# Performance work log

Hardware: AMD Instinct MI355X
Metric: run time of the kernel (lower is better)

## Reference

```python
import jax, jax.numpy as jnp
import numpy as np

BATCH, C, BOX = 8, 1, 160
N, L = 20, 20


def setup_inputs() -> dict:
    key = jax.random.key(0)
    k1, k2, k3 = jax.random.split(key, 3)
    x = jax.random.normal(k1, (BATCH, C, BOX, BOX), dtype=jnp.float32)
    basis = jax.random.normal(k2, (N, L, 2, BOX, BOX), dtype=jnp.float32)
    angles = jax.random.uniform(k3, (BATCH,), dtype=jnp.float32) * (2.0 * np.pi)
    return {"x": x, "basis": basis, "angles": angles}


def reference(x, basis, angles):
    # euclid2basis: linear basis projection (GEMM in disguise)
    # coeffs: [b, c, N, L, 2]
    coeffs = jnp.einsum('bcij,nlrij->bcnlr', x, basis)

    # rotate: complex rotation of angular modes, angle scaled by harmonic index l
    l_mult = jnp.arange(L, dtype=x.dtype)                  # [L]
    ang = angles[:, None, None, None] * l_mult             # [b, 1, 1, L]
    ca, sa = jnp.cos(ang), jnp.sin(ang)
    a = coeffs[..., 0] * ca + coeffs[..., 1] * sa
    b = coeffs[..., 1] * ca - coeffs[..., 0] * sa
    rot = jnp.stack([a, b], axis=-1)                       # [b, c, N, L, 2]

    # basis2euclid: reconstruction (transpose GEMM)
    out = jnp.einsum('bcnlr,nlrij->bcij', rot, basis)      # [b, c, H, W]
    return out
```

## Files before the change

### kernel.cpp

```cpp
#include <hip/hip_runtime.h>
#include <math.h>

#define BATCH   8
#define LDIM    20
#define PIX     25600
#define PIX4    6400
#define NLPAIRS 400
#define NLR     800

#define KSPLIT  20
#define SLICE   (PIX4 / KSPLIT)
#define WITER   (SLICE / 64)
#define BROWS   8

#define RPIX    64
#define RKS     8
#define RKLEN   (NLR / RKS)

__global__ __launch_bounds__(256) void proj_kernel(
    const float* __restrict__ x,
    const float* __restrict__ basis,
    float* __restrict__ part)
{
    const int tid   = threadIdx.x;
    const int lane  = tid & 63;
    const int wv    = tid >> 6;
    const int r0    = blockIdx.x * BROWS + wv * 2;
    const int kbase = blockIdx.y * SLICE;

    const float4* __restrict__ b0 = (const float4*)(basis + (size_t)r0 * PIX);
    const float4* __restrict__ b1 = (const float4*)(basis + (size_t)(r0 + 1) * PIX);
    const float4* __restrict__ x4 = (const float4*)x;

    float acc0[BATCH], acc1[BATCH];
    #pragma unroll
    for (int b = 0; b < BATCH; ++b) { acc0[b] = 0.0f; acc1[b] = 0.0f; }

    #pragma unroll
    for (int it = 0; it < WITER; ++it) {
        const int i = kbase + it * 64 + lane;
        float4 v0 = b0[i];
        float4 v1 = b1[i];
        #pragma unroll
        for (int b = 0; b < BATCH; ++b) {
            float4 xv = x4[(size_t)b * PIX4 + i];
            acc0[b] = fmaf(v0.x, xv.x, acc0[b]);
            acc0[b] = fmaf(v0.y, xv.y, acc0[b]);
            acc0[b] = fmaf(v0.z, xv.z, acc0[b]);
            acc0[b] = fmaf(v0.w, xv.w, acc0[b]);
            acc1[b] = fmaf(v1.x, xv.x, acc1[b]);
            acc1[b] = fmaf(v1.y, xv.y, acc1[b]);
            acc1[b] = fmaf(v1.z, xv.z, acc1[b]);
            acc1[b] = fmaf(v1.w, xv.w, acc1[b]);
        }
    }

    #pragma unroll
    for (int b = 0; b < BATCH; ++b) {
        #pragma unroll
        for (int off = 32; off > 0; off >>= 1) {
            acc0[b] += __shfl_down(acc0[b], off);
            acc1[b] += __shfl_down(acc1[b], off);
        }
    }

    if (lane == 0) {
        float* __restrict__ dst =
            part + ((size_t)blockIdx.y * NLR + r0) * BATCH;
        #pragma unroll
        for (int b = 0; b < BATCH; ++b) {
            dst[b]         = acc0[b];
            dst[BATCH + b] = acc1[b];
        }
    }
}

__global__ __launch_bounds__(256) void rotate_kernel(
    const float* __restrict__ part,
    const float* __restrict__ angles,
    float* __restrict__ rot)
{
    const int idx = blockIdx.x * 256 + threadIdx.x;
    const int nlr = idx >> 3;
    const int b   = idx & 7;

    float self = 0.0f, other = 0.0f;
    #pragma unroll
    for (int s = 0; s < KSPLIT; ++s) {
        self  += part[((size_t)s * NLR + nlr) * BATCH + b];
        other += part[((size_t)s * NLR + (nlr ^ 1)) * BATCH + b];
    }
    const int l = (nlr >> 1) % LDIM;
    float ca, sa;
    __sincosf(angles[b] * (float)l, &sa, &ca);
    rot[idx] = (nlr & 1) == 0 ? fmaf(self, ca, other * sa)
                              : fmaf(self, ca, -other * sa);
}

__global__ __launch_bounds__(512) void recon_kernel(
    const float* __restrict__ basis,
    const float* __restrict__ rot,
    float* __restrict__ out)
{
    __shared__ float rl[NLR * BATCH];
    __shared__ float red[RKS - 1][BATCH][RPIX];

    const int tid = threadIdx.x;

    for (int idx = tid; idx < NLR * BATCH; idx += 512)
        rl[idx] = rot[idx];
    __syncthreads();

    const int lane = tid & 63;
    const int ks   = tid >> 6;
    const int pix  = blockIdx.x * RPIX + lane;

    float acc[BATCH];
    #pragma unroll
    for (int b = 0; b < BATCH; ++b) acc[b] = 0.0f;

    const float* __restrict__ bp = basis + (size_t)(ks * RKLEN) * PIX + pix;
    const float* __restrict__ rp = &rl[(ks * RKLEN) * BATCH];

    #pragma unroll 10
    for (int k = 0; k < RKLEN; ++k) {
        float bv = bp[(size_t)k * PIX];
        float4 v0 = *(const float4*)&rp[k * BATCH];
        float4 v1 = *(const float4*)&rp[k * BATCH + 4];
        acc[0] = fmaf(bv, v0.x, acc[0]);
        acc[1] = fmaf(bv, v0.y, acc[1]);
        acc[2] = fmaf(bv, v0.z, acc[2]);
        acc[3] = fmaf(bv, v0.w, acc[3]);
        acc[4] = fmaf(bv, v1.x, acc[4]);
        acc[5] = fmaf(bv, v1.y, acc[5]);
        acc[6] = fmaf(bv, v1.z, acc[6]);
        acc[7] = fmaf(bv, v1.w, acc[7]);
    }

    if (ks > 0) {
        #pragma unroll
        for (int b = 0; b < BATCH; ++b)
            red[ks - 1][b][lane] = acc[b];
    }
    __syncthreads();

    if (ks == 0) {
        #pragma unroll
        for (int w = 0; w < RKS - 1; ++w)
            #pragma unroll
            for (int b = 0; b < BATCH; ++b)
                acc[b] += red[w][b][lane];
        #pragma unroll
        for (int b = 0; b < BATCH; ++b)
            out[(size_t)b * PIX + pix] = acc[b];
    }
}

extern "C" void kernel_launch(void* const* d_in, const int* in_sizes, int n_in,
                              void* d_out, int out_size, void* d_ws, size_t ws_size,
                              hipStream_t stream) {
    (void)in_sizes; (void)n_in; (void)ws_size; (void)out_size;

    const float* x      = (const float*)d_in[0];
    const float* basis  = (const float*)d_in[1];
    const float* angles = (const float*)d_in[2];
    float* out  = (float*)d_out;
    float* part = (float*)d_ws;
    float* rot  = part + (size_t)KSPLIT * NLR * BATCH;

    proj_kernel<<<dim3(NLR / BROWS, KSPLIT), dim3(256), 0, stream>>>(x, basis, part);
    rotate_kernel<<<dim3(NLR * BATCH / 256), dim3(256), 0, stream>>>(part, angles, rot);
    recon_kernel<<<dim3(PIX / RPIX), dim3(512), 0, stream>>>(basis, rot, out);
}
```

Before: 41.97 us.

## Fuse projection, rotation and reconstruction into one persistent kernel with grid barriers

Merges the three launches into one 400-block kernel, separating the phases with atomic-counter grid barriers whose counters are zeroed by a memset before launch. The projection now splits K into 4 sets instead of 20, so the rotate phase sums fewer partials, and reconstruction uses 4 waves per block instead of 8. The aim is to remove launch gaps and partial-sum traffic between kernels. In exchange there is barrier spin latency, an extra memset node, and a deadlock risk if not all 400 blocks are resident at once.

```diff
diff --git a/kernel.cpp b/kernel.cpp
--- a/kernel.cpp
+++ b/kernel.cpp
@@ -11,148 +11,175 @@
 #define KSPLIT  20
 #define SLICE   (PIX4 / KSPLIT)
 #define WITER   (SLICE / 64)
-#define BROWS   8
+#define NSETS   4
+#define NBLK    400
 
 #define RPIX    64
-#define RKS     8
+#define RKS     4
 #define RKLEN   (NLR / RKS)
 
-__global__ __launch_bounds__(256) void proj_kernel(
+#define PART_F  (NSETS * NLR * BATCH)
+#define ROT_F   (NLR * BATCH)
+#define CNT_OFF (PART_F + ROT_F)
+
+__device__ __forceinline__ void grid_barrier(unsigned* cnt, unsigned target) {
+    __syncthreads();
+    if (threadIdx.x == 0) {
+        __threadfence();
+        atomicAdd(cnt, 1u);
+        while (__hip_atomic_load(cnt, __ATOMIC_ACQUIRE,
+                                 __HIP_MEMORY_SCOPE_AGENT) < target)
+            __builtin_amdgcn_s_sleep(2);
+    }
+    __syncthreads();
+}
+
+__global__ __launch_bounds__(256) void fused_kernel(
     const float* __restrict__ x,
     const float* __restrict__ basis,
-    float* __restrict__ part)
-{
-    const int tid   = threadIdx.x;
-    const int lane  = tid & 63;
-    const int wv    = tid >> 6;
-    const int r0    = blockIdx.x * BROWS + wv * 2;
-    const int kbase = blockIdx.y * SLICE;
-
-    const float4* __restrict__ b0 = (const float4*)(basis + (size_t)r0 * PIX);
-    const float4* __restrict__ b1 = (const float4*)(basis + (size_t)(r0 + 1) * PIX);
-    const float4* __restrict__ x4 = (const float4*)x;
-
-    float acc0[BATCH], acc1[BATCH];
-    #pragma unroll
-    for (int b = 0; b < BATCH; ++b) { acc0[b] = 0.0f; acc1[b] = 0.0f; }
-
-    #pragma unroll
-    for (int it = 0; it < WITER; ++it) {
-        const int i = kbase + it * 64 + lane;
-        float4 v0 = b0[i];
-        float4 v1 = b1[i];
-        #pragma unroll
-        for (int b = 0; b < BATCH; ++b) {
-            float4 xv = x4[(size_t)b * PIX4 + i];
-            acc0[b] = fmaf(v0.x, xv.x, acc0[b]);
-            acc0[b] = fmaf(v0.y, xv.y, acc0[b]);
-            acc0[b] = fmaf(v0.z, xv.z, acc0[b]);
-            acc0[b] = fmaf(v0.w, xv.w, acc0[b]);
-            acc1[b] = fmaf(v1.x, xv.x, acc1[b]);
-            acc1[b] = fmaf(v1.y, xv.y, acc1[b]);
-            acc1[b] = fmaf(v1.z, xv.z, acc1[b]);
-            acc1[b] = fmaf(v1.w, xv.w, acc1[b]);
-        }
-    }
-
-    #pragma unroll
-    for (int b = 0; b < BATCH; ++b) {
-        #pragma unroll
-        for (int off = 32; off > 0; off >>= 1) {
-            acc0[b] += __shfl_down(acc0[b], off);
-            acc1[b] += __shfl_down(acc1[b], off);
-        }
-    }
-
-    if (lane == 0) {
-        float* __restrict__ dst =
-            part + ((size_t)blockIdx.y * NLR + r0) * BATCH;
-        #pragma unroll
-        for (int b = 0; b < BATCH; ++b) {
-            dst[b]         = acc0[b];
-            dst[BATCH + b] = acc1[b];
-        }
-    }
-}
-
-__global__ __launch_bounds__(256) void rotate_kernel(
-    const float* __restrict__ part,
     const float* __restrict__ angles,
-    float* __restrict__ rot)
-{
-    const int idx = blockIdx.x * 256 + threadIdx.x;
-    const int nlr = idx >> 3;
-    const int b   = idx & 7;
-
-    float self = 0.0f, other = 0.0f;
-    #pragma unroll
-    for (int s = 0; s < KSPLIT; ++s) {
-        self  += part[((size_t)s * NLR + nlr) * BATCH + b];
-        other += part[((size_t)s * NLR + (nlr ^ 1)) * BATCH + b];
-    }
-    const int l = (nlr >> 1) % LDIM;
-    float ca, sa;
-    __sincosf(angles[b] * (float)l, &sa, &ca);
-    rot[idx] = (nlr & 1) == 0 ? fmaf(self, ca, other * sa)
-                              : fmaf(self, ca, -other * sa);
-}
-
-__global__ __launch_bounds__(512) void recon_kernel(
-    const float* __restrict__ basis,
-    const float* __restrict__ rot,
-    float* __restrict__ out)
+    float* __restrict__ out,
+    float* __restrict__ ws)
 {
     __shared__ float rl[NLR * BATCH];
     __shared__ float red[RKS - 1][BATCH][RPIX];
 
-    const int tid = threadIdx.x;
-
-    for (int idx = tid; idx < NLR * BATCH; idx += 512)
-        rl[idx] = rot[idx];
-    __syncthreads();
-
+    float* __restrict__ part = ws;
+    float* __restrict__ rot  = ws + PART_F;
+    unsigned* __restrict__ cnt = (unsigned*)(ws + CNT_OFF);
+
+    const int tid  = threadIdx.x;
     const int lane = tid & 63;
-    const int ks   = tid >> 6;
-    const int pix  = blockIdx.x * RPIX + lane;
-
-    float acc[BATCH];
-    #pragma unroll
-    for (int b = 0; b < BATCH; ++b) acc[b] = 0.0f;
-
-    const float* __restrict__ bp = basis + (size_t)(ks * RKLEN) * PIX + pix;
-    const float* __restrict__ rp = &rl[(ks * RKLEN) * BATCH];
-
-    #pragma unroll 10
-    for (int k = 0; k < RKLEN; ++k) {
-        float bv = bp[(size_t)k * PIX];
-        float4 v0 = *(const float4*)&rp[k * BATCH];
-        float4 v1 = *(const float4*)&rp[k * BATCH + 4];
-        acc[0] = fmaf(bv, v0.x, acc[0]);
-        acc[1] = fmaf(bv, v0.y, acc[1]);
-        acc[2] = fmaf(bv, v0.z, acc[2]);
-        acc[3] = fmaf(bv, v0.w, acc[3]);
-        acc[4] = fmaf(bv, v1.x, acc[4]);
-        acc[5] = fmaf(bv, v1.y, acc[5]);
-        acc[6] = fmaf(bv, v1.z, acc[6]);
-        acc[7] = fmaf(bv, v1.w, acc[7]);
-    }
-
-    if (ks > 0) {
-        #pragma unroll
-        for (int b = 0; b < BATCH; ++b)
-            red[ks - 1][b][lane] = acc[b];
-    }
-    __syncthreads();
-
-    if (ks == 0) {
-        #pragma unroll
-        for (int w = 0; w < RKS - 1; ++w)
+    const int wv   = tid >> 6;
+    const int bid  = blockIdx.x;
+
+    {
+        const int wid = bid * 4 + wv;
+        const int rp  = wid & (NLPAIRS - 1);
+        const int rpm = wid % NLPAIRS;
+        const int set = wid / NLPAIRS;
+        (void)rp;
+        const int r0 = rpm * 2;
+
+        const float4* __restrict__ b0 = (const float4*)(basis + (size_t)r0 * PIX);
+        const float4* __restrict__ b1 = (const float4*)(basis + (size_t)(r0 + 1) * PIX);
+        const float4* __restrict__ x4 = (const float4*)x;
+
+        float acc0[BATCH], acc1[BATCH];
+        #pragma unroll
+        for (int b = 0; b < BATCH; ++b) { acc0[b] = 0.0f; acc1[b] = 0.0f; }
+
+        #pragma unroll
+        for (int k = 0; k < 5; ++k) {
+            const int kb = (set + 4 * k) * SLICE;
+            #pragma unroll
+            for (int it = 0; it < WITER; ++it) {
+                const int i = kb + it * 64 + lane;
+                float4 v0 = b0[i];
+                float4 v1 = b1[i];
+                #pragma unroll
+                for (int b = 0; b < BATCH; ++b) {
+                    float4 xv = x4[(size_t)b * PIX4 + i];
+                    acc0[b] = fmaf(v0.x, xv.x, acc0[b]);
+                    acc0[b] = fmaf(v0.y, xv.y, acc0[b]);
+                    acc0[b] = fmaf(v0.z, xv.z, acc0[b]);
+                    acc0[b] = fmaf(v0.w, xv.w, acc0[b]);
+                    acc1[b] = fmaf(v1.x, xv.x, acc1[b]);
+                    acc1[b] = fmaf(v1.y, xv.y, acc1[b]);
+                    acc1[b] = fmaf(v1.z, xv.z, acc1[b]);
+                    acc1[b] = fmaf(v1.w, xv.w, acc1[b]);
+                }
+            }
+        }
+
+        #pragma unroll
+        for (int b = 0; b < BATCH; ++b) {
+            #pragma unroll
+            for (int off = 32; off > 0; off >>= 1) {
+                acc0[b] += __shfl_down(acc0[b], off);
+                acc1[b] += __shfl_down(acc1[b], off);
+            }
+        }
+
+        if (lane == 0) {
+            float* __restrict__ dst = part + ((size_t)set * NLR + r0) * BATCH;
+            #pragma unroll
+            for (int b = 0; b < BATCH; ++b) {
+                dst[b]         = acc0[b];
+                dst[BATCH + b] = acc1[b];
+            }
+        }
+    }
+
+    grid_barrier(&cnt[0], NBLK);
+
+    {
+        const int idx = bid * 256 + tid;
+        if (idx < NLR * BATCH) {
+            const int nlr = idx >> 3;
+            const int b   = idx & 7;
+            float self = 0.0f, other = 0.0f;
+            #pragma unroll
+            for (int s = 0; s < NSETS; ++s) {
+                self  += part[((size_t)s * NLR + nlr) * BATCH + b];
+                other += part[((size_t)s * NLR + (nlr ^ 1)) * BATCH + b];
+            }
+            const int l = (nlr >> 1) % LDIM;
+            float ca, sa;
+            __sincosf(angles[b] * (float)l, &sa, &ca);
+            rot[idx] = (nlr & 1) == 0 ? fmaf(self, ca, other * sa)
+                                      : fmaf(self, ca, -other * sa);
+        }
+    }
+
+    grid_barrier(&cnt[1], NBLK);
+
+    {
+        for (int idx = tid; idx < NLR * BATCH; idx += 256)
+            rl[idx] = rot[idx];
+        __syncthreads();
+
+        const int pix = bid * RPIX + lane;
+
+        float acc[BATCH];
+        #pragma unroll
+        for (int b = 0; b < BATCH; ++b) acc[b] = 0.0f;
+
+        const float* __restrict__ bp = basis + (size_t)(wv * RKLEN) * PIX + pix;
+        const float* __restrict__ rp2 = &rl[(wv * RKLEN) * BATCH];
+
+        #pragma unroll 10
+        for (int k = 0; k < RKLEN; ++k) {
+            float bv = bp[(size_t)k * PIX];
+            float4 v0 = *(const float4*)&rp2[k * BATCH];
+            float4 v1 = *(const float4*)&rp2[k * BATCH + 4];
+            acc[0] = fmaf(bv, v0.x, acc[0]);
+            acc[1] = fmaf(bv, v0.y, acc[1]);
+            acc[2] = fmaf(bv, v0.z, acc[2]);
+            acc[3] = fmaf(bv, v0.w, acc[3]);
+            acc[4] = fmaf(bv, v1.x, acc[4]);
+            acc[5] = fmaf(bv, v1.y, acc[5]);
+            acc[6] = fmaf(bv, v1.z, acc[6]);
+            acc[7] = fmaf(bv, v1.w, acc[7]);
+        }
+
+        if (wv > 0) {
             #pragma unroll
             for (int b = 0; b < BATCH; ++b)
-                acc[b] += red[w][b][lane];
-        #pragma unroll
-        for (int b = 0; b < BATCH; ++b)
-            out[(size_t)b * PIX + pix] = acc[b];
+                red[wv - 1][b][lane] = acc[b];
+        }
+        __syncthreads();
+
+        if (wv == 0) {
+            #pragma unroll
+            for (int w = 0; w < RKS - 1; ++w)
+                #pragma unroll
+                for (int b = 0; b < BATCH; ++b)
+                    acc[b] += red[w][b][lane];
+            #pragma unroll
+            for (int b = 0; b < BATCH; ++b)
+                out[(size_t)b * PIX + pix] = acc[b];
+        }
     }
 }
 
@@ -164,11 +191,10 @@
     const float* x      = (const float*)d_in[0];
     const float* basis  = (const float*)d_in[1];
     const float* angles = (const float*)d_in[2];
-    float* out  = (float*)d_out;
-    float* part = (float*)d_ws;
-    float* rot  = part + (size_t)KSPLIT * NLR * BATCH;
-
-    proj_kernel<<<dim3(NLR / BROWS, KSPLIT), dim3(256), 0, stream>>>(x, basis, part);
-    rotate_kernel<<<dim3(NLR * BATCH / 256), dim3(256), 0, stream>>>(part, angles, rot);
-    recon_kernel<<<dim3(PIX / RPIX), dim3(512), 0, stream>>>(basis, rot, out);
+    float* out = (float*)d_out;
+    float* ws  = (float*)d_ws;
+
+    hipMemsetAsync((char*)d_ws + CNT_OFF * sizeof(float), 0, 2 * sizeof(unsigned), stream);
+
+    fused_kernel<<<dim3(NBLK), dim3(256), 0, stream>>>(x, basis, angles, out, ws);
 }
```

New measurement: 128.3 us. 206% more time.

## Restructure projection as per-pixel-tile partials with butterfly transpose-reduce

Applied to the files above, without the earlier changes.

The projection kernel now gives each block a 256-pixel tile and 32 basis rows. Each wave computes 64 (row, batch) dot products over 4 pixels per lane, then reduces them with a recursive-halving shuffle butterfly so that each lane ends up holding one finished sum. This replaces 64 separate full-wave reductions and writes partials fully coalesced. The cost is moved to the rotate kernel, which must now sum 100 partials per output instead of 20, and the 64-entry register array raises register pressure.

```diff
diff --git a/kernel.cpp b/kernel.cpp
--- a/kernel.cpp
+++ b/kernel.cpp
@@ -4,14 +4,12 @@
 #define BATCH   8
 #define LDIM    20
 #define PIX     25600
-#define PIX4    6400
 #define NLPAIRS 400
 #define NLR     800
 
-#define KSPLIT  20
-#define SLICE   (PIX4 / KSPLIT)
-#define WITER   (SLICE / 64)
-#define BROWS   8
+#define PPB     256
+#define NPX     (PIX / PPB)
+#define RSPLIT  25
 
 #define RPIX    64
 #define RKS     8
@@ -25,54 +23,47 @@
     const int tid   = threadIdx.x;
     const int lane  = tid & 63;
     const int wv    = tid >> 6;
-    const int r0    = blockIdx.x * BROWS + wv * 2;
-    const int kbase = blockIdx.y * SLICE;
+    const int p     = blockIdx.x;
+    const int rbase = blockIdx.y * 32 + wv * 8;
+    const int px    = p * PPB + lane * 4;
 
-    const float4* __restrict__ b0 = (const float4*)(basis + (size_t)r0 * PIX);
-    const float4* __restrict__ b1 = (const float4*)(basis + (size_t)(r0 + 1) * PIX);
-    const float4* __restrict__ x4 = (const float4*)x;
+    float4 xv[BATCH];
+    #pragma unroll
+    for (int b = 0; b < BATCH; ++b)
+        xv[b] = *(const float4*)(x + (size_t)b * PIX + px);
 
-    float acc0[BATCH], acc1[BATCH];
+    float4 bv[8];
     #pragma unroll
-    for (int b = 0; b < BATCH; ++b) { acc0[b] = 0.0f; acc1[b] = 0.0f; }
+    for (int r = 0; r < 8; ++r)
+        bv[r] = *(const float4*)(basis + (size_t)(rbase + r) * PIX + px);
+
+    float v[64];
+    #pragma unroll
+    for (int r = 0; r < 8; ++r)
+        #pragma unroll
+        for (int b = 0; b < BATCH; ++b)
+            v[r * 8 + b] = fmaf(bv[r].w, xv[b].w,
+                           fmaf(bv[r].z, xv[b].z,
+                           fmaf(bv[r].y, xv[b].y, bv[r].x * xv[b].x)));
 
     #pragma unroll
-    for (int it = 0; it < WITER; ++it) {
-        const int i = kbase + it * 64 + lane;
-        float4 v0 = b0[i];
-        float4 v1 = b1[i];
+    for (int k = 0; k < 6; ++k) {
+        const int m  = 1 << k;
+        const int kb = (lane >> k) & 1;
+        const int n  = 64 >> k;
         #pragma unroll
-        for (int b = 0; b < BATCH; ++b) {
-            float4 xv = x4[(size_t)b * PIX4 + i];
-            acc0[b] = fmaf(v0.x, xv.x, acc0[b]);
-            acc0[b] = fmaf(v0.y, xv.y, acc0[b]);
-            acc0[b] = fmaf(v0.z, xv.z, acc0[b]);
-            acc0[b] = fmaf(v0.w, xv.w, acc0[b]);
-            acc1[b] = fmaf(v1.x, xv.x, acc1[b]);
-            acc1[b] = fmaf(v1.y, xv.y, acc1[b]);
-            acc1[b] = fmaf(v1.z, xv.z, acc1[b]);
-            acc1[b] = fmaf(v1.w, xv.w, acc1[b]);
+        for (int j = 0; j < 32; ++j) {
+            if (j < n / 2) {
+                float a    = v[2 * j];
+                float c    = v[2 * j + 1];
+                float send = kb ? a : c;
+                float keep = kb ? c : a;
+                v[j] = keep + __shfl_xor(send, m);
+            }
         }
     }
 
-    #pragma unroll
-    for (int b = 0; b < BATCH; ++b) {
-        #pragma unroll
-        for (int off = 32; off > 0; off >>= 1) {
-            acc0[b] += __shfl_down(acc0[b], off);
-            acc1[b] += __shfl_down(acc1[b], off);
-        }
-    }
-
-    if (lane == 0) {
-        float* __restrict__ dst =
-            part + ((size_t)blockIdx.y * NLR + r0) * BATCH;
-        #pragma unroll
-        for (int b = 0; b < BATCH; ++b) {
-            dst[b]         = acc0[b];
-            dst[BATCH + b] = acc1[b];
-        }
-    }
+    part[(size_t)p * (NLR * BATCH) + blockIdx.y * 256 + wv * 64 + lane] = v[0];
 }
 
 __global__ __launch_bounds__(256) void rotate_kernel(
@@ -84,12 +75,12 @@
     const int nlr = idx >> 3;
     const int b   = idx & 7;
 
-    float self = 0.0f, other = 0.0f;
-    #pragma unroll
-    for (int s = 0; s < KSPLIT; ++s) {
-        self  += part[((size_t)s * NLR + nlr) * BATCH + b];
-        other += part[((size_t)s * NLR + (nlr ^ 1)) * BATCH + b];
-    }
+    float self = 0.0f;
+    for (int p = 0; p < NPX; ++p)
+        self += part[(size_t)p * (NLR * BATCH) + idx];
+
+    float other = __shfl_xor(self, 8);
+
     const int l = (nlr >> 1) % LDIM;
     float ca, sa;
     __sincosf(angles[b] * (float)l, &sa, &ca);
@@ -124,17 +115,17 @@
 
     #pragma unroll 10
     for (int k = 0; k < RKLEN; ++k) {
-        float bv = bp[(size_t)k * PIX];
+        float bvv = bp[(size_t)k * PIX];
         float4 v0 = *(const float4*)&rp[k * BATCH];
         float4 v1 = *(const float4*)&rp[k * BATCH + 4];
-        acc[0] = fmaf(bv, v0.x, acc[0]);
-        acc[1] = fmaf(bv, v0.y, acc[1]);
-        acc[2] = fmaf(bv, v0.z, acc[2]);
-        acc[3] = fmaf(bv, v0.w, acc[3]);
-        acc[4] = fmaf(bv, v1.x, acc[4]);
-        acc[5] = fmaf(bv, v1.y, acc[5]);
-        acc[6] = fmaf(bv, v1.z, acc[6]);
-        acc[7] = fmaf(bv, v1.w, acc[7]);
+        acc[0] = fmaf(bvv, v0.x, acc[0]);
+        acc[1] = fmaf(bvv, v0.y, acc[1]);
+        acc[2] = fmaf(bvv, v0.z, acc[2]);
+        acc[3] = fmaf(bvv, v0.w, acc[3]);
+        acc[4] = fmaf(bvv, v1.x, acc[4]);
+        acc[5] = fmaf(bvv, v1.y, acc[5]);
+        acc[6] = fmaf(bvv, v1.z, acc[6]);
+        acc[7] = fmaf(bvv, v1.w, acc[7]);
     }
 
     if (ks > 0) {
@@ -166,9 +157,9 @@
     const float* angles = (const float*)d_in[2];
     float* out  = (float*)d_out;
     float* part = (float*)d_ws;
-    float* rot  = part + (size_t)KSPLIT * NLR * BATCH;
+    float* rot  = part + (size_t)NPX * NLR * BATCH;
 
-    proj_kernel<<<dim3(NLR / BROWS, KSPLIT), dim3(256), 0, stream>>>(x, basis, part);
+    proj_kernel<<<dim3(NPX, RSPLIT), dim3(256), 0, stream>>>(x, basis, part);
     rotate_kernel<<<dim3(NLR * BATCH / 256), dim3(256), 0, stream>>>(part, angles, rot);
     recon_kernel<<<dim3(PIX / RPIX), dim3(512), 0, stream>>>(basis, rot, out);
 }
```

Result: no change. 42.50 us (+1.2%).
